# Kernel tuning notes

Hardware: AMD Instinct MI355X
Metric: run time of the kernel (lower is better)

## Reference

```python
import jax, jax.numpy as jnp
import numpy as np

N_NODES = 200000
N_EDGES = 2000000
B = 1024
SEQ = 1000
EMB = 128
VOC = 26  # num_features_xt + 1
BN_EPS = 1e-5


def setup_inputs() -> dict:
    key = jax.random.key(0)
    ks = jax.random.split(key, 40)
    f32 = jnp.float32
    def nrm(k, shp, s=0.05):
        return jax.random.normal(k, shp, dtype=f32) * s
    inp = {}
    inp['x'] = jax.random.normal(ks[0], (N_NODES, 78), dtype=f32)
    inp['edge_index'] = jax.random.randint(ks[1], (2, N_EDGES), 0, N_NODES, dtype=jnp.int32)
    inp['batch'] = jnp.sort(jax.random.randint(ks[2], (N_NODES,), 0, B, dtype=jnp.int32))
    inp['target'] = jax.random.randint(ks[3], (B, SEQ), 0, VOC, dtype=jnp.int32)
    # GIN layer 1 (78 -> 32 -> 32)
    inp['W1a'] = nrm(ks[4], (78, 32)); inp['b1a'] = jnp.zeros((32,), f32)
    inp['W2a'] = nrm(ks[5], (32, 32)); inp['b2a'] = jnp.zeros((32,), f32)
    inp['g1'] = jnp.ones((32,), f32); inp['be1'] = jnp.zeros((32,), f32)
    # GIN layers 2-5 stacked
    inp['Ws1'] = nrm(ks[6], (4, 32, 32)); inp['bs1'] = jnp.zeros((4, 32), f32)
    inp['Ws2'] = nrm(ks[7], (4, 32, 32)); inp['bs2'] = jnp.zeros((4, 32), f32)
    inp['gs'] = jnp.ones((4, 32), f32); inp['bes'] = jnp.zeros((4, 32), f32)
    # drug head
    inp['fc1xd_W'] = nrm(ks[8], (32, 128)); inp['fc1xd_b'] = jnp.zeros((128,), f32)
    # protein branch
    inp['emb'] = nrm(ks[9], (VOC, EMB), 1.0)
    inp['convW'] = nrm(ks[10], (32, SEQ, 8))  # Conv1d(1000, 32, k=8): (O, I, K)
    inp['convb'] = jnp.zeros((32,), f32)
    inp['fcxt_W'] = nrm(ks[11], (32 * 121, 128)); inp['fcxt_b'] = jnp.zeros((128,), f32)
    # joint head
    inp['fc1_W'] = nrm(ks[12], (256, 1024)); inp['fc1_b'] = jnp.zeros((1024,), f32)
    inp['fc2_W'] = nrm(ks[13], (1024, 256)); inp['fc2_b'] = jnp.zeros((256,), f32)
    inp['out_W'] = nrm(ks[14], (256, 1)); inp['out_b'] = jnp.zeros((1,), f32)
    return inp


def _bn(h, g, b):
    m = h.mean(axis=0)
    v = h.var(axis=0)
    return (h - m) * jax.lax.rsqrt(v + BN_EPS) * g + b


def _gin(x, src, dst, W1, b1, W2, b2):
    # GIN aggregation (eps=0): (1+eps)*x + sum_{j->i} x_j, then 2-layer MLP
    agg = jax.ops.segment_sum(x[src], dst, num_segments=x.shape[0]) + x
    return jnp.maximum(agg @ W1 + b1, 0.0) @ W2 + b2


def reference(x, edge_index, batch, target, W1a, b1a, W2a, b2a, g1, be1,
              Ws1, bs1, Ws2, bs2, gs, bes, fc1xd_W, fc1xd_b, emb, convW, convb,
              fcxt_W, fcxt_b, fc1_W, fc1_b, fc2_W, fc2_b, out_W, out_b):
    relu = jax.nn.relu
    src, dst = edge_index[0], edge_index[1]
    h = _bn(relu(_gin(x, src, dst, W1a, b1a, W2a, b2a)), g1, be1)
    for i in range(4):
        h = _bn(relu(_gin(h, src, dst, Ws1[i], bs1[i], Ws2[i], bs2[i])), gs[i], bes[i])
    nb = target.shape[0]
    pooled = jax.ops.segment_sum(h, batch, num_segments=nb)  # [B, 32]
    xd = relu(pooled @ fc1xd_W + fc1xd_b)  # dropout: identity at eval
    # protein branch: embedding [B, 1000, 128] -> Conv1d over C=1000, L=128
    xe = emb[target]
    conv = jax.lax.conv_general_dilated(xe, convW, (1,), 'VALID',
                                        dimension_numbers=('NCH', 'OIH', 'NCH'))
    conv = conv + convb[None, :, None]  # [B, 32, 121]
    xt = conv.reshape(nb, 32 * 121) @ fcxt_W + fcxt_b
    xc = jnp.concatenate([xd, xt], axis=1)
    xc = relu(xc @ fc1_W + fc1_b)
    xc = relu(xc @ fc2_W + fc2_b)
    return xc @ out_W + out_b
```

## Files before the change

kernel.cpp:

```cpp
#include <hip/hip_runtime.h>

#define N_NODES 200000
#define N_EDGES 2000000
#define BATCH   1024
#define SEQ     1000
#define EMBD    128
#define VOC     26
#define BN_EPS  1e-5f
#define NB      128
#define NBUK    1563
#define CAP     2048
#define STG     8192
#define BPT     7



__global__ __launch_bounds__(256, 1) void k_bscatter(const int* __restrict__ ei,
                                                     int* __restrict__ gcnt,
                                                     unsigned int* __restrict__ epk) {
    __shared__ int lcnt[NBUK];
    __shared__ int lpos[NBUK];
    __shared__ int sbase[NBUK];
    __shared__ int ssum[256];
    __shared__ int2 stage[STG];
    int tid = threadIdx.x;
    int e0 = blockIdx.x * STG;
    int m = min(STG, N_EDGES - e0);
    for (int i = tid; i < NBUK; i += 256) lcnt[i] = 0;
    __syncthreads();
    for (int i = tid; i < m; i += 256) {
        int d = ei[N_EDGES + e0 + i];
        atomicAdd(&lcnt[d >> 7], 1);
    }
    __syncthreads();
    int v[BPT]; int s0 = 0; int bb = tid * BPT;
#pragma unroll
    for (int k = 0; k < BPT; k++) {
        int idx = bb + k;
        v[k] = (idx < NBUK) ? lcnt[idx] : 0;
        s0 += v[k];
    }
    ssum[tid] = s0;
    __syncthreads();
    for (int off = 1; off < 256; off <<= 1) {
        int x = (tid >= off) ? ssum[tid - off] : 0;
        __syncthreads();
        ssum[tid] += x;
        __syncthreads();
    }
    int run = ssum[tid] - s0;
#pragma unroll
    for (int k = 0; k < BPT; k++) {
        int idx = bb + k;
        if (idx < NBUK) { lpos[idx] = run; run += v[k]; }
    }
    __syncthreads();
    for (int i = tid; i < NBUK; i += 256) {
        int c = lcnt[i];
        if (c > 0) {
            int gb = atomicAdd(&gcnt[i], c);
            sbase[i] = gb - lpos[i];
        }
    }
    __syncthreads();
    for (int i = tid; i < m; i += 256) {
        int s = ei[e0 + i];
        int d = ei[N_EDGES + e0 + i];
        int p = atomicAdd(&lpos[d >> 7], 1);
        stage[p] = make_int2(s, d);
    }
    __syncthreads();
    for (int i = tid; i < m; i += 256) {
        int2 ed = stage[i];
        int b = ed.y >> 7;
        int slot = sbase[b] + i;
        if (slot < CAP)
            epk[(size_t)b * CAP + slot] = ((unsigned int)ed.x << 8) | (unsigned int)(ed.y & 127);
    }
}

__global__ __launch_bounds__(256, 8) void k_bsort(const int* __restrict__ gcnt,
                                                  unsigned int* __restrict__ epk) {
    __shared__ unsigned int stg[CAP];
    __shared__ unsigned int srt[CAP];
    __shared__ int cnt[NB];
    __shared__ int pos[NB];
    int b = blockIdx.x, tid = threadIdx.x;
    int fill = min(gcnt[b], CAP);
    unsigned int* slab = epk + (size_t)b * CAP;
    for (int i = tid; i < fill; i += 256) stg[i] = slab[i];
    if (tid < NB) cnt[tid] = 0;
    __syncthreads();
    for (int i = tid; i < fill; i += 256) atomicAdd(&cnt[stg[i] & (NB - 1)], 1);
    __syncthreads();
    if (tid < NB) pos[tid] = cnt[tid];
    __syncthreads();
    for (int off = 1; off < NB; off <<= 1) {
        int x = (tid < NB && tid >= off) ? pos[tid - off] : 0;
        __syncthreads();
        if (tid < NB) pos[tid] += x;
        __syncthreads();
    }
    if (tid < NB) cnt[tid] = pos[tid] - cnt[tid];
    __syncthreads();
    for (int i = tid; i < fill; i += 256) {
        int p = atomicAdd(&cnt[stg[i] & (NB - 1)], 1);
        srt[p] = stg[i];
    }
    __syncthreads();
    for (int i = tid; i < fill; i += 256) slab[i] = srt[i];
}


__global__ __launch_bounds__(128) void k_proj78(const float* __restrict__ x,
                                                const float* __restrict__ W,
                                                float* __restrict__ y) {
    __shared__ __align__(16) float xs[128 * 78];
    __shared__ __align__(16) float ws[78 * 32];
    int tid = threadIdx.x;
    int base = blockIdx.x * 128;
    for (int i = tid; i < 78 * 32; i += 128) ws[i] = W[i];
    int cnt = min(128, N_NODES - base);
    for (int i = tid; i < cnt * 78; i += 128) xs[i] = x[(size_t)base * 78 + i];
    __syncthreads();
    int n = base + tid;
    if (tid >= cnt) return;
    float acc[32];
#pragma unroll
    for (int j = 0; j < 32; j++) acc[j] = 0.f;
    const float* xr = &xs[tid * 78];
    for (int c = 0; c < 78; c++) {
        float xv = xr[c];
        const float4* w4 = (const float4*)&ws[c * 32];
#pragma unroll
        for (int j4 = 0; j4 < 8; j4++) {
            float4 w = w4[j4];
            acc[j4 * 4 + 0] += xv * w.x; acc[j4 * 4 + 1] += xv * w.y;
            acc[j4 * 4 + 2] += xv * w.z; acc[j4 * 4 + 3] += xv * w.w;
        }
    }
    float4* yo = (float4*)&y[(size_t)n * 32];
#pragma unroll
    for (int j4 = 0; j4 < 8; j4++)
        yo[j4] = make_float4(acc[j4*4], acc[j4*4+1], acc[j4*4+2], acc[j4*4+3]);
}

__global__ __launch_bounds__(256) void k_proj32(const float* __restrict__ hbuf,
                                                const float* __restrict__ stats,
                                                const float* __restrict__ g,
                                                const float* __restrict__ be,
                                                const float* __restrict__ W,
                                                float* __restrict__ y) {
    __shared__ __align__(16) float ts[256 * 33];
    __shared__ __align__(16) float ws[1024];
    __shared__ float as_[32], cs_[32];
    int tid = threadIdx.x, base = blockIdx.x * 256;
    for (int i = tid; i < 1024; i += 256) ws[i] = W[i];
    if (tid < 32) {
        float inv_n = 1.f / (float)N_NODES;
        float m = stats[tid] * inv_n;
        float var = stats[32 + tid] * inv_n - m * m;
        float a = g[tid] * rsqrtf(var + BN_EPS);
        as_[tid] = a;
        cs_[tid] = be[tid] - m * a;
    }
    int cnt = min(256, N_NODES - base);
    for (int i = tid; i < cnt * 32; i += 256) ts[(i >> 5) * 33 + (i & 31)] = hbuf[(size_t)base * 32 + i];
    __syncthreads();
    if (tid >= cnt) return;
    float acc[32];
#pragma unroll
    for (int j = 0; j < 32; j++) acc[j] = 0.f;
    for (int c = 0; c < 32; c++) {
        float zv = ts[tid * 33 + c] * as_[c] + cs_[c];
        const float4* w4 = (const float4*)&ws[c * 32];
#pragma unroll
        for (int j4 = 0; j4 < 8; j4++) {
            float4 w = w4[j4];
            acc[j4*4+0] += zv * w.x; acc[j4*4+1] += zv * w.y;
            acc[j4*4+2] += zv * w.z; acc[j4*4+3] += zv * w.w;
        }
    }
    int n = base + tid;
    float4* yo = (float4*)&y[(size_t)n * 32];
#pragma unroll
    for (int j4 = 0; j4 < 8; j4++)
        yo[j4] = make_float4(acc[j4*4], acc[j4*4+1], acc[j4*4+2], acc[j4*4+3]);
}

__global__ __launch_bounds__(256, 5) void k_gmlp(const float* __restrict__ y,
                                                 const int* __restrict__ gcnt,
                                                 const unsigned int* __restrict__ epk,
                                                 const float* __restrict__ b1,
                                                 const float* __restrict__ W2,
                                                 const float* __restrict__ b2,
                                                 float* __restrict__ h,
                                                 float* __restrict__ stats) {
    __shared__ __align__(16) float ts[NB * 33];
    __shared__ __align__(16) float ws[1024];
    __shared__ __align__(16) unsigned int es[CAP];
    __shared__ float b1s[32], b2s[32];
    __shared__ float sp[8][32], sq[8][32];
    int tid = threadIdx.x, base = blockIdx.x * NB;
    for (int i = tid; i < 1024; i += 256) ws[i] = W2[i];
    if (tid < 32) { b1s[tid] = b1[tid]; b2s[tid] = b2[tid]; }
    int cnt = min(NB, N_NODES - base);
    int fill = min(gcnt[blockIdx.x], CAP);
    int pfill = (fill + 127) & ~127;
    for (int i = tid; i < fill; i += 256) es[i] = epk[(size_t)blockIdx.x * CAP + i];
    for (int i = fill + tid; i < pfill; i += 256) es[i] = 128u;
    for (int i = tid; i < cnt * 32; i += 256) ts[(i >> 5) * 33 + (i & 31)] = y[(size_t)base * 32 + i];
    __syncthreads();
    {
        int hw = tid >> 5, c = tid & 31;
        for (int se = hw * 16; se < pfill; se += 128) {
            float rr[16]; int dd[16];
#pragma unroll
            for (int k = 0; k < 16; k++) {
                unsigned int p = es[se + k];
                rr[k] = y[(size_t)(p >> 8) * 32 + c];
                dd[k] = (int)(p & 255u);
            }
            float acc = rr[0]; int cur = dd[0];
#pragma unroll
            for (int k = 1; k < 16; k++) {
                if (dd[k] == cur) acc += rr[k];
                else { atomicAdd(&ts[cur * 33 + c], acc); acc = rr[k]; cur = dd[k]; }
            }
            if (cur < 128) atomicAdd(&ts[cur * 33 + c], acc);
        }
    }
    __syncthreads();
    float t[32];
    if (tid < cnt) {
        float z[32];
#pragma unroll
        for (int c = 0; c < 32; c++) z[c] = fmaxf(ts[tid * 33 + c] + b1s[c], 0.f);
        float acc[32];
#pragma unroll
        for (int j = 0; j < 32; j++) acc[j] = b2s[j];
        for (int c = 0; c < 32; c++) {
            float zv = z[c];
            const float4* w4 = (const float4*)&ws[c * 32];
#pragma unroll
            for (int j4 = 0; j4 < 8; j4++) {
                float4 w = w4[j4];
                acc[j4*4+0] += zv * w.x; acc[j4*4+1] += zv * w.y;
                acc[j4*4+2] += zv * w.z; acc[j4*4+3] += zv * w.w;
            }
        }
#pragma unroll
        for (int j = 0; j < 32; j++) t[j] = fmaxf(acc[j], 0.f);
    } else {
#pragma unroll
        for (int j = 0; j < 32; j++) t[j] = 0.f;
    }
    __syncthreads();
    if (tid < NB) {
#pragma unroll
        for (int c = 0; c < 32; c++) ts[tid * 33 + c] = t[c];
    }
    __syncthreads();
    {
        int c = tid & 31, g = tid >> 5;
        float s = 0.f, q = 0.f;
        for (int r = g * 16; r < g * 16 + 16; r++) { float v = ts[r * 33 + c]; s += v; q += v * v; }
        sp[g][c] = s; sq[g][c] = q;
    }
    __syncthreads();
    if (tid < 32) {
        float s = 0.f, q = 0.f;
#pragma unroll
        for (int g = 0; g < 8; g++) { s += sp[g][tid]; q += sq[g][tid]; }
        atomicAdd(&stats[tid], s);
        atomicAdd(&stats[32 + tid], q);
    }
    for (int i = tid; i < cnt * 32; i += 256) h[(size_t)base * 32 + i] = ts[(i >> 5) * 33 + (i & 31)];
}

__device__ __forceinline__ int lbound(const int* __restrict__ b, int val) {
    int lo = 0, hi = N_NODES;
    while (lo < hi) { int mid = (lo + hi) >> 1; if (b[mid] < val) lo = mid + 1; else hi = mid; }
    return lo;
}

__global__ __launch_bounds__(256) void k_pool(const float* __restrict__ h,
                                              const int* __restrict__ batch,
                                              const float* __restrict__ stats,
                                              const float* __restrict__ gw,
                                              const float* __restrict__ be,
                                              float* __restrict__ pooled) {
    __shared__ float sp[8][32];
    int g = blockIdx.x;
    int start = lbound(batch, g), end = lbound(batch, g + 1);
    int c = threadIdx.x & 31, gg = threadIdx.x >> 5;
    float acc = 0.f;
    for (int r = start + gg; r < end; r += 8) acc += h[(size_t)r * 32 + c];
    sp[gg][c] = acc;
    __syncthreads();
    if (threadIdx.x < 32) {
        int j = threadIdx.x;
        float s = 0.f;
#pragma unroll
        for (int k = 0; k < 8; k++) s += sp[k][j];
        float inv_n = 1.f / (float)N_NODES;
        float m = stats[j] * inv_n;
        float var = stats[32 + j] * inv_n - m * m;
        float a = gw[j] * rsqrtf(var + BN_EPS);
        float cc = be[j] - m * a;
        pooled[g * 32 + j] = a * s + cc * (float)(end - start);
    }
}

__global__ __launch_bounds__(256) void k_xd(const float* __restrict__ pooled,
                                            const float* __restrict__ W,
                                            const float* __restrict__ b,
                                            float* __restrict__ xc) {
    int t = blockIdx.x * 256 + threadIdx.x;
    int row = t >> 7, col = t & 127;
    if (row >= BATCH) return;
    float acc = b[col];
    for (int k = 0; k < 32; k++) acc += pooled[row * 32 + k] * W[k * 128 + col];
    xc[row * 256 + col] = fmaxf(acc, 0.f);
}


__global__ __launch_bounds__(256) void k_trw(const float* __restrict__ convW,
                                             float* __restrict__ Wt) {
    int t = blockIdx.x * 256 + threadIdx.x;
    if (t >= 32 * SEQ * 8) return;
    int o = t / (SEQ * 8), r = t % (SEQ * 8), i = r >> 3, k = r & 7;
    Wt[i * 256 + o * 8 + k] = convW[t];
}

__global__ __launch_bounds__(256) void k_prot1(const int* __restrict__ target,
                                               const float* __restrict__ Wt,
                                               float* __restrict__ Sg) {
    __shared__ int tv[SEQ];
    __shared__ int pos_[SEQ];
    __shared__ int off_[VOC + 1];
    __shared__ int cur_[VOC];
    int tid = threadIdx.x, b = blockIdx.x;
    for (int i = tid; i < SEQ; i += 256) tv[i] = target[(size_t)b * SEQ + i];
    if (tid < VOC + 1) off_[tid] = 0;
    __syncthreads();
    for (int i = tid; i < SEQ; i += 256) atomicAdd(&off_[tv[i] + 1], 1);
    __syncthreads();
    if (tid == 0) for (int v = 1; v <= VOC; v++) off_[v] += off_[v - 1];
    __syncthreads();
    if (tid < VOC) cur_[tid] = off_[tid];
    __syncthreads();
    for (int i = tid; i < SEQ; i += 256) {
        int p = atomicAdd(&cur_[tv[i]], 1);
        pos_[p] = i;
    }
    __syncthreads();
    for (int v = 0; v < VOC; v++) {
        int e0 = off_[v], e1 = off_[v + 1];
        float a0 = 0.f, a1 = 0.f, a2 = 0.f, a3 = 0.f, a4 = 0.f, a5 = 0.f, a6 = 0.f, a7 = 0.f;
        int k = e0;
        for (; k + 8 <= e1; k += 8) {
            a0 += Wt[(size_t)pos_[k + 0] * 256 + tid];
            a1 += Wt[(size_t)pos_[k + 1] * 256 + tid];
            a2 += Wt[(size_t)pos_[k + 2] * 256 + tid];
            a3 += Wt[(size_t)pos_[k + 3] * 256 + tid];
            a4 += Wt[(size_t)pos_[k + 4] * 256 + tid];
            a5 += Wt[(size_t)pos_[k + 5] * 256 + tid];
            a6 += Wt[(size_t)pos_[k + 6] * 256 + tid];
            a7 += Wt[(size_t)pos_[k + 7] * 256 + tid];
        }
        for (; k < e1; k++) a0 += Wt[(size_t)pos_[k] * 256 + tid];
        Sg[((size_t)b * VOC + v) * 256 + tid] = ((a0 + a1) + (a2 + a3)) + ((a4 + a5) + (a6 + a7));
    }
}

__global__ __launch_bounds__(256, 4) void k_prot2(const float* __restrict__ Sg,
                                                  const float* __restrict__ emb,
                                                  const float* __restrict__ convb,
                                                  float* __restrict__ conv) {
    __shared__ __align__(16) float S[VOC * 256];
    __shared__ __align__(16) float embs[VOC * EMBD];
    int tid = threadIdx.x, b = blockIdx.x;
    for (int i = tid; i < VOC * 256; i += 256) S[i] = Sg[(size_t)b * (VOC * 256) + i];
    for (int i = tid; i < VOC * EMBD; i += 256) embs[i] = emb[i];
    __syncthreads();
    int og = tid >> 6, lt = tid & 63;
    bool has2 = (lt < 57);
    float acc0[8], acc1[8];
#pragma unroll
    for (int oi = 0; oi < 8; oi++) {
        float bb = convb[og * 8 + oi];
        acc0[oi] = bb; acc1[oi] = bb;
    }
    for (int v = 0; v < VOC; v++) {
        float er0[8], er1[8];
#pragma unroll
        for (int k = 0; k < 8; k++) er0[k] = embs[v * EMBD + lt + k];
#pragma unroll
        for (int k = 0; k < 8; k++) er1[k] = has2 ? embs[v * EMBD + lt + 64 + k] : 0.f;
        const float* sv = &S[v * 256 + og * 64];
#pragma unroll
        for (int oi = 0; oi < 8; oi++) {
#pragma unroll
            for (int k = 0; k < 8; k++) {
                float s = sv[oi * 8 + k];
                acc0[oi] += s * er0[k];
                acc1[oi] += s * er1[k];
            }
        }
    }
#pragma unroll
    for (int oi = 0; oi < 8; oi++) {
        int o = og * 8 + oi;
        conv[((size_t)b * 32 + o) * 121 + lt] = acc0[oi];
        if (has2) conv[((size_t)b * 32 + o) * 121 + lt + 64] = acc1[oi];
    }
}


__global__ __launch_bounds__(256) void k_init_bias(float* __restrict__ C, int ldc, int coff,
                                                   const float* __restrict__ bias, int nb) {
    int t = blockIdx.x * 256 + threadIdx.x;
    int row = t / nb, col = t % nb;
    if (row >= BATCH) return;
    C[row * ldc + coff + col] = bias[col];
}

template <int ROWS, bool ATOMIC, bool RELU>
__global__ __launch_bounds__(256, 3) void k_gemm(const float* __restrict__ A, int lda,
                                                 const float* __restrict__ W, int ldw,
                                                 const float* __restrict__ bias,
                                                 float* __restrict__ C, int ldc, int coff,
                                                 int mtc, int ntc, int klen) {
    constexpr int P  = ROWS + 4;
    constexpr int HR = ROWS / 2;
    constexpr int TPR = 256 / ROWS;
    __shared__ __align__(16) float As[64 * P];
    __shared__ __align__(16) float Ws[64 * 128];
    int bid = blockIdx.x;
    int mt = bid % mtc, nt = (bid / mtc) % ntc, ks = bid / (mtc * ntc);
    int row0 = mt * ROWS, col0 = nt * 128, k0 = ks * klen;
    int tid = threadIdx.x;
    int j = tid & 127, rh = tid >> 7;
    float acc[HR];
#pragma unroll
    for (int m = 0; m < HR; m++) acc[m] = (ATOMIC || bias == nullptr) ? 0.f : bias[col0 + j];
    int lr = tid / TPR, lk = tid % TPR;
    for (int kc = 0; kc < klen; kc += 64) {
        int cc = min(64, klen - kc);
        __syncthreads();
        for (int kk = lk; kk < cc; kk += TPR)
            As[kk * P + lr] = A[(size_t)(row0 + lr) * lda + k0 + kc + kk];
        for (int i = tid; i < cc * 32; i += 256) {
            int r = i >> 5, c4 = (i & 31) << 2;
            *(float4*)&Ws[r * 128 + c4] =
                *(const float4*)&W[(size_t)(k0 + kc + r) * ldw + col0 + c4];
        }
        __syncthreads();
#pragma unroll 4
        for (int kk = 0; kk < cc; kk++) {
            float w = Ws[kk * 128 + j];
            const float4* a4 = (const float4*)&As[kk * P + rh * HR];
#pragma unroll
            for (int m4 = 0; m4 < HR / 4; m4++) {
                float4 a = a4[m4];
                acc[m4*4+0] += a.x * w; acc[m4*4+1] += a.y * w;
                acc[m4*4+2] += a.z * w; acc[m4*4+3] += a.w * w;
            }
        }
    }
#pragma unroll
    for (int m = 0; m < HR; m++) {
        int row = row0 + rh * HR + m;
        float* p = &C[(size_t)row * ldc + coff + col0 + j];
        if (ATOMIC) atomicAdd(p, acc[m]);
        else { float v = acc[m]; if (RELU) v = fmaxf(v, 0.f); *p = v; }
    }
}

__global__ __launch_bounds__(256) void k_out(const float* __restrict__ xc2,
                                             const float* __restrict__ W,
                                             const float* __restrict__ b,
                                             float* __restrict__ out) {
    int gt = blockIdx.x * 256 + threadIdx.x;
    int wid = gt >> 6, lane = gt & 63;
    if (wid >= BATCH) return;
    float4 xv = ((const float4*)&xc2[(size_t)wid * 256])[lane];
    float4 wv = ((const float4*)W)[lane];
    float s = fmaxf(xv.x, 0.f) * wv.x + fmaxf(xv.y, 0.f) * wv.y +
              fmaxf(xv.z, 0.f) * wv.z + fmaxf(xv.w, 0.f) * wv.w;
    for (int off = 32; off; off >>= 1) s += __shfl_down(s, off, 64);
    if (lane == 0) out[wid] = s + b[0];
}


extern "C" void kernel_launch(void* const* d_in, const int* in_sizes, int n_in,
                              void* d_out, int out_size, void* d_ws, size_t ws_size,
                              hipStream_t stream) {
    const float* x      = (const float*)d_in[0];
    const int*   ei     = (const int*)d_in[1];
    const int*   batch  = (const int*)d_in[2];
    const int*   target = (const int*)d_in[3];
    const float* W1a = (const float*)d_in[4];
    const float* b1a = (const float*)d_in[5];
    const float* W2a = (const float*)d_in[6];
    const float* b2a = (const float*)d_in[7];
    const float* g1  = (const float*)d_in[8];
    const float* be1 = (const float*)d_in[9];
    const float* Ws1 = (const float*)d_in[10];
    const float* bs1 = (const float*)d_in[11];
    const float* Ws2 = (const float*)d_in[12];
    const float* bs2 = (const float*)d_in[13];
    const float* gs  = (const float*)d_in[14];
    const float* bes = (const float*)d_in[15];
    const float* fc1xd_W = (const float*)d_in[16];
    const float* fc1xd_b = (const float*)d_in[17];
    const float* emb   = (const float*)d_in[18];
    const float* convW = (const float*)d_in[19];
    const float* convb = (const float*)d_in[20];
    const float* fcxt_W = (const float*)d_in[21];
    const float* fcxt_b = (const float*)d_in[22];
    const float* fc1_W = (const float*)d_in[23];
    const float* fc1_b = (const float*)d_in[24];
    const float* fc2_W = (const float*)d_in[25];
    const float* fc2_b = (const float*)d_in[26];
    const float* out_W = (const float*)d_in[27];
    const float* out_b = (const float*)d_in[28];
    float* out = (float*)d_out;

    char* ws = (char*)d_ws;
    size_t off = 0;
    auto alloc = [&](size_t bytes) { char* p = ws + off; off += (bytes + 4095) & ~(size_t)4095; return p; };
    float* y    = (float*)alloc((size_t)N_NODES * 32 * 4);
    float* h    = (float*)alloc((size_t)N_NODES * 32 * 4);
    unsigned int* epk = (unsigned int*)alloc((size_t)NBUK * CAP * 4);
    int* gcnt = (int*)alloc((size_t)NBUK * 4);
    float* stats  = (float*)alloc(5 * 64 * 4);
    float* pooled = (float*)alloc(BATCH * 32 * 4);
    float* xc  = (float*)alloc(BATCH * 256 * 4);
    float* xc1 = (float*)alloc(BATCH * 1024 * 4);
    float* xc2 = (float*)alloc(BATCH * 256 * 4);
    float* Wt  = (float*)alloc(SEQ * 256 * 4);
    float* Sg   = h;
    float* conv = y;

    hipMemsetAsync(stats, 0, 5 * 64 * 4, stream);
    hipMemsetAsync(gcnt, 0, (size_t)NBUK * 4, stream);

    const int PROJ78_G = (N_NODES + 127) / 128;
    const int NODE256  = (N_NODES + 255) / 256;
    const int PART_G   = (N_EDGES + STG - 1) / STG;

    k_bscatter<<<PART_G, 256, 0, stream>>>(ei, gcnt, epk);
    k_bsort<<<NBUK, 256, 0, stream>>>(gcnt, epk);

    k_proj78<<<PROJ78_G, 128, 0, stream>>>(x, W1a, y);
    k_gmlp<<<NBUK, 256, 0, stream>>>(y, gcnt, epk, b1a, W2a, b2a, h, stats);
    for (int i = 0; i < 4; i++) {
        const float* gg = (i == 0) ? g1 : gs + (i - 1) * 32;
        const float* bb = (i == 0) ? be1 : bes + (i - 1) * 32;
        k_proj32<<<NODE256, 256, 0, stream>>>(h, stats + i * 64, gg, bb, Ws1 + i * 1024, y);
        k_gmlp<<<NBUK, 256, 0, stream>>>(y, gcnt, epk, bs1 + i * 32, Ws2 + i * 1024,
                                         bs2 + i * 32, h, stats + (i + 1) * 64);
    }
    k_pool<<<BATCH, 256, 0, stream>>>(h, batch, stats + 4 * 64, gs + 3 * 32, bes + 3 * 32, pooled);
    k_xd<<<(BATCH * 128) / 256, 256, 0, stream>>>(pooled, fc1xd_W, fc1xd_b, xc);
    k_trw<<<(32 * SEQ * 8) / 256, 256, 0, stream>>>(convW, Wt);
    k_prot1<<<BATCH, 256, 0, stream>>>(target, Wt, Sg);
    k_prot2<<<BATCH, 256, 0, stream>>>(Sg, emb, convb, conv);
    k_init_bias<<<(BATCH * 128) / 256, 256, 0, stream>>>(xc, 256, 128, fcxt_b, 128);
    k_gemm<32, true, false><<<32 * 1 * 16, 256, 0, stream>>>(conv, 3872, fcxt_W, 128, nullptr,
                                                             xc, 256, 128, 32, 1, 242);
    k_gemm<32, false, true><<<32 * 8 * 1, 256, 0, stream>>>(xc, 256, fc1_W, 1024, fc1_b,
                                                            xc1, 1024, 0, 32, 8, 256);
    k_init_bias<<<(BATCH * 256) / 256, 256, 0, stream>>>(xc2, 256, 0, fc2_b, 256);
    k_gemm<32, true, false><<<32 * 2 * 4, 256, 0, stream>>>(xc1, 1024, fc2_W, 256, nullptr,
                                                            xc2, 256, 0, 32, 2, 256);
    k_out<<<(BATCH * 64) / 256, 256, 0, stream>>>(xc2, out_W, out_b, out);
}
```

Before: 1.107 ms.

## Fold BN and first GIN linear into aggregation kernel using node degrees

Removes the separate per-layer projection kernel. The BatchNorm affine and W1 matmul now run after aggregation: the raw normalized-input h is aggregated, multiplied by the BN-scaled W1, and a degree-weighted bias term (deg+1)*(c·W1) is added. Node in-degrees are recorded during the bucket sort. Gather batches go from 16 to 32 edges, with destinations packed into bytes, and h buffers are ping-ponged. This saves one full node-array read/write pass per layer, at the cost of more registers (occupancy hint lowered to 4) and extra setup per block.

```diff
diff --git a/kernel.cpp b/kernel.cpp
--- a/kernel.cpp
+++ b/kernel.cpp
@@ -80,7 +80,8 @@
 }
 
 __global__ __launch_bounds__(256, 8) void k_bsort(const int* __restrict__ gcnt,
-                                                  unsigned int* __restrict__ epk) {
+                                                  unsigned int* __restrict__ epk,
+                                                  int* __restrict__ deg) {
     __shared__ unsigned int stg[CAP];
     __shared__ unsigned int srt[CAP];
     __shared__ int cnt[NB];
@@ -93,7 +94,7 @@
     __syncthreads();
     for (int i = tid; i < fill; i += 256) atomicAdd(&cnt[stg[i] & (NB - 1)], 1);
     __syncthreads();
-    if (tid < NB) pos[tid] = cnt[tid];
+    if (tid < NB) { pos[tid] = cnt[tid]; deg[b * NB + tid] = cnt[tid]; }
     __syncthreads();
     for (int off = 1; off < NB; off <<= 1) {
         int x = (tid < NB && tid >= off) ? pos[tid - off] : 0;
@@ -145,87 +146,77 @@
         yo[j4] = make_float4(acc[j4*4], acc[j4*4+1], acc[j4*4+2], acc[j4*4+3]);
 }
 
-__global__ __launch_bounds__(256) void k_proj32(const float* __restrict__ hbuf,
-                                                const float* __restrict__ stats,
-                                                const float* __restrict__ g,
-                                                const float* __restrict__ be,
-                                                const float* __restrict__ W,
-                                                float* __restrict__ y) {
-    __shared__ __align__(16) float ts[256 * 33];
-    __shared__ __align__(16) float ws[1024];
-    __shared__ float as_[32], cs_[32];
-    int tid = threadIdx.x, base = blockIdx.x * 256;
-    for (int i = tid; i < 1024; i += 256) ws[i] = W[i];
-    if (tid < 32) {
-        float inv_n = 1.f / (float)N_NODES;
-        float m = stats[tid] * inv_n;
-        float var = stats[32 + tid] * inv_n - m * m;
-        float a = g[tid] * rsqrtf(var + BN_EPS);
-        as_[tid] = a;
-        cs_[tid] = be[tid] - m * a;
-    }
-    int cnt = min(256, N_NODES - base);
-    for (int i = tid; i < cnt * 32; i += 256) ts[(i >> 5) * 33 + (i & 31)] = hbuf[(size_t)base * 32 + i];
-    __syncthreads();
-    if (tid >= cnt) return;
-    float acc[32];
-#pragma unroll
-    for (int j = 0; j < 32; j++) acc[j] = 0.f;
-    for (int c = 0; c < 32; c++) {
-        float zv = ts[tid * 33 + c] * as_[c] + cs_[c];
-        const float4* w4 = (const float4*)&ws[c * 32];
-#pragma unroll
-        for (int j4 = 0; j4 < 8; j4++) {
-            float4 w = w4[j4];
-            acc[j4*4+0] += zv * w.x; acc[j4*4+1] += zv * w.y;
-            acc[j4*4+2] += zv * w.z; acc[j4*4+3] += zv * w.w;
-        }
-    }
-    int n = base + tid;
-    float4* yo = (float4*)&y[(size_t)n * 32];
-#pragma unroll
-    for (int j4 = 0; j4 < 8; j4++)
-        yo[j4] = make_float4(acc[j4*4], acc[j4*4+1], acc[j4*4+2], acc[j4*4+3]);
-}
-
-__global__ __launch_bounds__(256, 5) void k_gmlp(const float* __restrict__ y,
+template <bool FOLD>
+__global__ __launch_bounds__(256, 4) void k_gmlp(const float* __restrict__ hin,
                                                  const int* __restrict__ gcnt,
                                                  const unsigned int* __restrict__ epk,
+                                                 const int* __restrict__ deg,
+                                                 const float* __restrict__ stats,
+                                                 const float* __restrict__ g,
+                                                 const float* __restrict__ be,
+                                                 const float* __restrict__ W1,
                                                  const float* __restrict__ b1,
                                                  const float* __restrict__ W2,
                                                  const float* __restrict__ b2,
                                                  float* __restrict__ h,
-                                                 float* __restrict__ stats) {
+                                                 float* __restrict__ statsOut) {
     __shared__ __align__(16) float ts[NB * 33];
-    __shared__ __align__(16) float ws[1024];
+    __shared__ __align__(16) float w2s[1024];
+    __shared__ __align__(16) float wc[FOLD ? 1024 : 4];
     __shared__ __align__(16) unsigned int es[CAP];
+    __shared__ float as_[FOLD ? 32 : 1], cs_[FOLD ? 32 : 1], cv[FOLD ? 32 : 1];
     __shared__ float b1s[32], b2s[32];
     __shared__ float sp[8][32], sq[8][32];
     int tid = threadIdx.x, base = blockIdx.x * NB;
-    for (int i = tid; i < 1024; i += 256) ws[i] = W2[i];
+    for (int i = tid; i < 1024; i += 256) w2s[i] = W2[i];
     if (tid < 32) { b1s[tid] = b1[tid]; b2s[tid] = b2[tid]; }
+    if constexpr (FOLD) {
+        if (tid < 32) {
+            float inv_n = 1.f / (float)N_NODES;
+            float m = stats[tid] * inv_n;
+            float var = stats[32 + tid] * inv_n - m * m;
+            float a = g[tid] * rsqrtf(var + BN_EPS);
+            as_[tid] = a;
+            cs_[tid] = be[tid] - m * a;
+        }
+        __syncthreads();
+        for (int i = tid; i < 1024; i += 256) wc[i] = as_[i >> 5] * W1[i];
+        if (tid < 32) {
+            float s = 0.f;
+            for (int k = 0; k < 32; k++) s += cs_[k] * W1[k * 32 + tid];
+            cv[tid] = s;
+        }
+    }
     int cnt = min(NB, N_NODES - base);
     int fill = min(gcnt[blockIdx.x], CAP);
-    int pfill = (fill + 127) & ~127;
+    int pfill = (fill + 255) & ~255;
+    int dg = 0;
+    if (FOLD && tid < cnt) dg = deg[base + tid];
     for (int i = tid; i < fill; i += 256) es[i] = epk[(size_t)blockIdx.x * CAP + i];
     for (int i = fill + tid; i < pfill; i += 256) es[i] = 128u;
-    for (int i = tid; i < cnt * 32; i += 256) ts[(i >> 5) * 33 + (i & 31)] = y[(size_t)base * 32 + i];
+    for (int i = tid; i < cnt * 32; i += 256) ts[(i >> 5) * 33 + (i & 31)] = hin[(size_t)base * 32 + i];
     __syncthreads();
     {
         int hw = tid >> 5, c = tid & 31;
-        for (int se = hw * 16; se < pfill; se += 128) {
-            float rr[16]; int dd[16];
-#pragma unroll
-            for (int k = 0; k < 16; k++) {
-                unsigned int p = es[se + k];
-                rr[k] = y[(size_t)(p >> 8) * 32 + c];
-                dd[k] = (int)(p & 255u);
+        for (int se = hw * 32; se < pfill; se += 256) {
+            float rr[32]; unsigned int dpk[8];
+#pragma unroll
+            for (int k4 = 0; k4 < 8; k4++) {
+                unsigned int dp = 0;
+#pragma unroll
+                for (int q = 0; q < 4; q++) {
+                    unsigned int p = es[se + k4 * 4 + q];
+                    rr[k4 * 4 + q] = hin[(size_t)(p >> 8) * 32 + c];
+                    dp |= (p & 255u) << (8 * q);
+                }
+                dpk[k4] = dp;
             }
-            float acc = rr[0]; int cur = dd[0];
-#pragma unroll
-            for (int k = 1; k < 16; k++) {
-                if (dd[k] == cur) acc += rr[k];
-                else { atomicAdd(&ts[cur * 33 + c], acc); acc = rr[k]; cur = dd[k]; }
+            float acc = rr[0]; int cur = (int)(dpk[0] & 255u);
+#pragma unroll
+            for (int k = 1; k < 32; k++) {
+                int d = (int)((dpk[k >> 2] >> (8 * (k & 3))) & 255u);
+                if (d == cur) acc += rr[k];
+                else { atomicAdd(&ts[cur * 33 + c], acc); acc = rr[k]; cur = d; }
             }
             if (cur < 128) atomicAdd(&ts[cur * 33 + c], acc);
         }
@@ -233,15 +224,31 @@
     __syncthreads();
     float t[32];
     if (tid < cnt) {
-        float z[32];
-#pragma unroll
-        for (int c = 0; c < 32; c++) z[c] = fmaxf(ts[tid * 33 + c] + b1s[c], 0.f);
+        float v[32];
+        if constexpr (FOLD) {
+            float dgf = (float)(dg + 1);
+#pragma unroll
+            for (int j = 0; j < 32; j++) v[j] = b1s[j] + dgf * cv[j];
+            for (int c = 0; c < 32; c++) {
+                float av = ts[tid * 33 + c];
+                const float4* w4 = (const float4*)&wc[c * 32];
+#pragma unroll
+                for (int j4 = 0; j4 < 8; j4++) {
+                    float4 w = w4[j4];
+                    v[j4*4+0] += av * w.x; v[j4*4+1] += av * w.y;
+                    v[j4*4+2] += av * w.z; v[j4*4+3] += av * w.w;
+                }
+            }
+        } else {
+#pragma unroll
+            for (int c = 0; c < 32; c++) v[c] = ts[tid * 33 + c] + b1s[c];
+        }
         float acc[32];
 #pragma unroll
         for (int j = 0; j < 32; j++) acc[j] = b2s[j];
         for (int c = 0; c < 32; c++) {
-            float zv = z[c];
-            const float4* w4 = (const float4*)&ws[c * 32];
+            float zv = fmaxf(v[c], 0.f);
+            const float4* w4 = (const float4*)&w2s[c * 32];
 #pragma unroll
             for (int j4 = 0; j4 < 8; j4++) {
                 float4 w = w4[j4];
@@ -262,18 +269,18 @@
     }
     __syncthreads();
     {
-        int c = tid & 31, g = tid >> 5;
+        int c = tid & 31, gg = tid >> 5;
         float s = 0.f, q = 0.f;
-        for (int r = g * 16; r < g * 16 + 16; r++) { float v = ts[r * 33 + c]; s += v; q += v * v; }
-        sp[g][c] = s; sq[g][c] = q;
+        for (int r = gg * 16; r < gg * 16 + 16; r++) { float vv = ts[r * 33 + c]; s += vv; q += vv * vv; }
+        sp[gg][c] = s; sq[gg][c] = q;
     }
     __syncthreads();
     if (tid < 32) {
         float s = 0.f, q = 0.f;
 #pragma unroll
-        for (int g = 0; g < 8; g++) { s += sp[g][tid]; q += sq[g][tid]; }
-        atomicAdd(&stats[tid], s);
-        atomicAdd(&stats[32 + tid], q);
+        for (int gg = 0; gg < 8; gg++) { s += sp[gg][tid]; q += sq[gg][tid]; }
+        atomicAdd(&statsOut[tid], s);
+        atomicAdd(&statsOut[32 + tid], q);
     }
     for (int i = tid; i < cnt * 32; i += 256) h[(size_t)base * 32 + i] = ts[(i >> 5) * 33 + (i & 31)];
 }
@@ -541,6 +548,7 @@
     float* xc1 = (float*)alloc(BATCH * 1024 * 4);
     float* xc2 = (float*)alloc(BATCH * 256 * 4);
     float* Wt  = (float*)alloc(SEQ * 256 * 4);
+    int* deg  = (int*)alloc((size_t)NBUK * NB * 4);
     float* Sg   = h;
     float* conv = y;
 
@@ -548,22 +556,24 @@
     hipMemsetAsync(gcnt, 0, (size_t)NBUK * 4, stream);
 
     const int PROJ78_G = (N_NODES + 127) / 128;
-    const int NODE256  = (N_NODES + 255) / 256;
     const int PART_G   = (N_EDGES + STG - 1) / STG;
 
     k_bscatter<<<PART_G, 256, 0, stream>>>(ei, gcnt, epk);
-    k_bsort<<<NBUK, 256, 0, stream>>>(gcnt, epk);
+    k_bsort<<<NBUK, 256, 0, stream>>>(gcnt, epk, deg);
 
     k_proj78<<<PROJ78_G, 128, 0, stream>>>(x, W1a, y);
-    k_gmlp<<<NBUK, 256, 0, stream>>>(y, gcnt, epk, b1a, W2a, b2a, h, stats);
+    k_gmlp<false><<<NBUK, 256, 0, stream>>>(y, gcnt, epk, deg, nullptr, nullptr, nullptr,
+                                            nullptr, b1a, W2a, b2a, h, stats);
+    float* hin = h; float* hout = y;
     for (int i = 0; i < 4; i++) {
         const float* gg = (i == 0) ? g1 : gs + (i - 1) * 32;
         const float* bb = (i == 0) ? be1 : bes + (i - 1) * 32;
-        k_proj32<<<NODE256, 256, 0, stream>>>(h, stats + i * 64, gg, bb, Ws1 + i * 1024, y);
-        k_gmlp<<<NBUK, 256, 0, stream>>>(y, gcnt, epk, bs1 + i * 32, Ws2 + i * 1024,
-                                         bs2 + i * 32, h, stats + (i + 1) * 64);
-    }
-    k_pool<<<BATCH, 256, 0, stream>>>(h, batch, stats + 4 * 64, gs + 3 * 32, bes + 3 * 32, pooled);
+        k_gmlp<true><<<NBUK, 256, 0, stream>>>(hin, gcnt, epk, deg, stats + i * 64, gg, bb,
+                                               Ws1 + i * 1024, bs1 + i * 32, Ws2 + i * 1024,
+                                               bs2 + i * 32, hout, stats + (i + 1) * 64);
+        float* tmp = hin; hin = hout; hout = tmp;
+    }
+    k_pool<<<BATCH, 256, 0, stream>>>(hin, batch, stats + 4 * 64, gs + 3 * 32, bes + 3 * 32, pooled);
     k_xd<<<(BATCH * 128) / 256, 256, 0, stream>>>(pooled, fc1xd_W, fc1xd_b, xc);
     k_trw<<<(32 * SEQ * 8) / 256, 256, 0, stream>>>(convW, Wt);
     k_prot1<<<BATCH, 256, 0, stream>>>(target, Wt, Sg);
```

Result: faster. 1.062 ms (-4.0%).
